# Performance work log

Hardware: AMD Instinct MI355X
Metric: run time of the kernel (lower is better)

Reference implementation:

```python
import jax, jax.numpy as jnp
import numpy as np

B, S, D, H = 2, 2048, 1024, 16
DH = D // H  # head_dim = 64


def setup_inputs() -> dict:
    key = jax.random.key(0)
    ks = jax.random.split(key, 10)
    inp = {
        "query": jax.random.normal(ks[0], (B, S, D), jnp.float32),
        "key": jax.random.normal(ks[1], (B, S, D), jnp.float32),
        "value": jax.random.normal(ks[2], (B, S, D), jnp.float32),
        "mask": jnp.ones((B, S), jnp.int32),
        # per-head q/k/v projections stacked over the head axis [H, D, DH]
        "Wq": jax.random.normal(ks[3], (H, D, DH), jnp.float32) * 0.02,
        "bq": jnp.zeros((H, DH), jnp.float32),
        "Wk": jax.random.normal(ks[4], (H, D, DH), jnp.float32) * 0.02,
        "bk": jnp.zeros((H, DH), jnp.float32),
        "Wv": jax.random.normal(ks[5], (H, D, DH), jnp.float32) * 0.02,
        "bv": jnp.zeros((H, DH), jnp.float32),
        # output projection fc: Linear(D, D)
        "Wo": jax.random.normal(ks[6], (D, D), jnp.float32) * 0.02,
        "bo": jnp.zeros((D,), jnp.float32),
    }
    return inp


def reference(query, key, value, mask, Wq, bq, Wk, bk, Wv, bv, Wo, bo):
    scale = 1.0 / jnp.sqrt(jnp.asarray(DH, query.dtype))
    # batched per-head projections: [B,S,D] x [H,D,DH] -> [B,H,S,DH]
    q = jnp.einsum('bsd,hde->bhse', query, Wq) + bq[None, :, None, :]
    k = jnp.einsum('bsd,hde->bhse', key, Wk) + bk[None, :, None, :]
    v = jnp.einsum('bsd,hde->bhse', value, Wv) + bv[None, :, None, :]
    # scaled dot-product attention scores [B,H,Sq,Sk]
    scores = jnp.einsum('bhqe,bhke->bhqk', q, k) * scale
    scores = jnp.where(mask[:, None, None, :] == 0, jnp.asarray(-1e9, scores.dtype), scores)
    attn = jax.nn.softmax(scores, axis=-1)
    ctx = jnp.einsum('bhqk,bhke->bhqe', attn, v)          # [B,H,S,DH]
    ctx = ctx.transpose(0, 2, 1, 3).reshape(query.shape[0], -1, H * DH)  # concat heads
    return ctx @ Wo + bo
```

## Files before the change

### kernel.cpp

```cpp
#include <hip/hip_runtime.h>
#include <stdint.h>
#include <math.h>


typedef __attribute__((ext_vector_type(8))) short short8;
typedef __attribute__((ext_vector_type(4))) float floatx4;

#define LOG2E 1.44269504088896340736f

__device__ __forceinline__ unsigned short f32_bf16(float f) {
  union { float f; unsigned u; } c; c.f = f;
  return (unsigned short)((c.u + 0x7FFFu + ((c.u >> 16) & 1u)) >> 16);
}
__device__ __forceinline__ float bf16_f32(unsigned short u) {
  union { unsigned u; float f; } c; c.u = ((unsigned)u) << 16;
  return c.f;
}
__device__ __forceinline__ void gld16(const void* g, void* l) {
  __builtin_amdgcn_global_load_lds((const __attribute__((address_space(1))) void*)g,
                                   (__attribute__((address_space(3))) void*)l, 16, 0, 0);
}


__global__ __launch_bounds__(256) void cvt3_kernel(
    const float* __restrict__ a, const float* __restrict__ b, const float* __restrict__ c,
    unsigned short* __restrict__ oa, unsigned short* __restrict__ ob, unsigned short* __restrict__ oc,
    const int* __restrict__ mask, float* __restrict__ mb, int n4) {
  int i = blockIdx.x * 256 + threadIdx.x;
  if (blockIdx.y == 0 && blockIdx.x < 16) {
    int j = blockIdx.x * 256 + threadIdx.x;
    mb[j] = (mask[j] == 0) ? (-1.0e9f * LOG2E) : 0.0f;
  }
  if (i >= n4) return;
  const float* in; unsigned short* out;
  if (blockIdx.y == 0) { in = a; out = oa; }
  else if (blockIdx.y == 1) { in = b; out = ob; }
  else { in = c; out = oc; }
  float4 v = reinterpret_cast<const float4*>(in)[i];
  ushort4 o;
  o.x = f32_bf16(v.x); o.y = f32_bf16(v.y); o.z = f32_bf16(v.z); o.w = f32_bf16(v.w);
  reinterpret_cast<ushort4*>(out)[i] = o;
}

__global__ __launch_bounds__(256) void transpose_w_kernel(
    const float* __restrict__ w0, const float* __restrict__ w1, const float* __restrict__ w2,
    const float* __restrict__ wo,
    unsigned short* __restrict__ o0, unsigned short* __restrict__ o1, unsigned short* __restrict__ o2,
    unsigned short* __restrict__ oo) {
  __shared__ float t[32][33];
  const int tx = threadIdx.x & 31, ty = threadIdx.x >> 5;
  const int zb = blockIdx.z;
  const float* in; unsigned short* out; int R, C, z, r0, c0;
  if (zb < 48) {
    if (blockIdx.y >= 2) return;
    const int sel = zb >> 4; z = zb & 15;
    in = (sel == 0) ? w0 : (sel == 1) ? w1 : w2;
    out = (sel == 0) ? o0 : (sel == 1) ? o1 : o2;
    R = 1024; C = 64;
  } else {
    in = wo; out = oo; R = 1024; C = 1024; z = 0;
  }
  r0 = blockIdx.x * 32; c0 = blockIdx.y * 32;
  const float* inp = in + (size_t)z * R * C;
  #pragma unroll
  for (int j = 0; j < 4; ++j)
    t[ty + j * 8][tx] = inp[(size_t)(r0 + ty + j * 8) * C + c0 + tx];
  __syncthreads();
  #pragma unroll
  for (int j = 0; j < 4; ++j)
    out[((size_t)z * C + c0 + ty + j * 8) * R + r0 + tx] = f32_bf16(t[tx][ty + j * 8]);
}


__device__ __forceinline__ void gemm_core(
    const unsigned short* __restrict__ A, const unsigned short* __restrict__ Bt,
    int K, int blockM, int blockN,
    unsigned short* As, unsigned short* Bs, floatx4 acc[4][4]) {
  const int tid = threadIdx.x;
  const int w = tid >> 6;
  const int lane = tid & 63;
  const int quad = lane >> 4, l15 = lane & 15;
  const int wm = w & 1, wn = w >> 1;
  const int srow = lane >> 2;
  const int scol = (lane & 3) * 8;

  #pragma unroll
  for (int mi = 0; mi < 4; ++mi)
    #pragma unroll
    for (int ni = 0; ni < 4; ++ni)
      acc[mi][ni] = (floatx4){0.f, 0.f, 0.f, 0.f};

  const unsigned short* Arow = A + (size_t)blockM * K;
  const unsigned short* Brow = Bt + (size_t)blockN * K;

  for (int k0 = 0; k0 < K; k0 += 32) {
    #pragma unroll
    for (int i = 0; i < 2; ++i) {
      int row = w * 32 + i * 16;
      gld16(Arow + (size_t)(row + srow) * K + k0 + scol, As + row * 32);
      gld16(Brow + (size_t)(row + srow) * K + k0 + scol, Bs + row * 32);
    }
    __syncthreads();
    short8 bf[4];
    #pragma unroll
    for (int ni = 0; ni < 4; ++ni)
      bf[ni] = *(const short8*)(Bs + (wn * 64 + ni * 16 + l15) * 32 + quad * 8);
    #pragma unroll
    for (int mi = 0; mi < 4; ++mi) {
      short8 af = *(const short8*)(As + (wm * 64 + mi * 16 + l15) * 32 + quad * 8);
      #pragma unroll
      for (int ni = 0; ni < 4; ++ni)
        acc[mi][ni] = __builtin_amdgcn_mfma_f32_16x16x32_bf16(af, bf[ni], acc[mi][ni], 0, 0, 0);
    }
    __syncthreads();
  }
}

__global__ __launch_bounds__(256) void gemm_proj_kernel(
    const unsigned short* __restrict__ qin, const unsigned short* __restrict__ kin,
    const unsigned short* __restrict__ vin,
    const unsigned short* __restrict__ WqT, const unsigned short* __restrict__ WkT,
    const unsigned short* __restrict__ WvT,
    const float* __restrict__ bq, const float* __restrict__ bk, const float* __restrict__ bv,
    unsigned short* __restrict__ Qp, unsigned short* __restrict__ Kp,
    unsigned short* __restrict__ Vt) {
  __shared__ unsigned short As[128 * 32];
  __shared__ unsigned short Bs[128 * 32];
  const int z = blockIdx.y, bx = blockIdx.x;
  const unsigned short *A, *Bt;
  const float* bias;
  int blockM, blockN;
  if (z < 2) {
    blockN = (bx & 7) * 128; blockM = (bx >> 3) * 128;
    A = z ? kin : qin; Bt = z ? WkT : WqT; bias = z ? bk : bq;
  } else {
    blockM = (bx & 7) * 128; blockN = (bx >> 3) * 128;
    A = WvT; Bt = vin; bias = bv;
  }
  floatx4 acc[4][4];
  gemm_core(A, Bt, 1024, blockM, blockN, As, Bs, acc);

  const int tid = threadIdx.x, w = tid >> 6, lane = tid & 63;
  const int quad = lane >> 4, l15 = lane & 15;
  const int wm = w & 1, wn = w >> 1;

  if (z < 2) {
    unsigned short* outp = z ? Kp : Qp;
    #pragma unroll
    for (int mi = 0; mi < 4; ++mi)
      #pragma unroll
      for (int ni = 0; ni < 4; ++ni) {
        const int n = blockN + wn * 64 + ni * 16 + l15;
        const int h = n >> 6, e = n & 63;
        const float bvv = bias[n];
        #pragma unroll
        for (int r = 0; r < 4; ++r) {
          const int m = blockM + wm * 64 + mi * 16 + quad * 4 + r;
          const int b = m >> 11, s = m & 2047;
          outp[(((size_t)b * 16 + h) * 2048 + s) * 64 + e] = f32_bf16(acc[mi][ni][r] + bvv);
        }
      }
  } else {
    #pragma unroll
    for (int mi = 0; mi < 4; ++mi) {
      float br[4];
      #pragma unroll
      for (int r = 0; r < 4; ++r)
        br[r] = bias[blockM + wm * 64 + mi * 16 + quad * 4 + r];
      #pragma unroll
      for (int ni = 0; ni < 4; ++ni) {
        const int n = blockN + wn * 64 + ni * 16 + l15;
        const int b = n >> 11, s = n & 2047;
        #pragma unroll
        for (int r = 0; r < 4; ++r) {
          const int m = blockM + wm * 64 + mi * 16 + quad * 4 + r;
          const int h = m >> 6, e = m & 63;
          Vt[(((size_t)b * 16 + h) * 64 + e) * 2048 + s] = f32_bf16(acc[mi][ni][r] + br[r]);
        }
      }
    }
  }
}

__global__ __launch_bounds__(256) void gemm_out_kernel(
    const unsigned short* __restrict__ A, const unsigned short* __restrict__ Bt,
    const float* __restrict__ bias, float* __restrict__ out, int K, int N) {
  __shared__ unsigned short As[128 * 32];
  __shared__ unsigned short Bs[64 * 32];
  const int tid = threadIdx.x;
  const int w = tid >> 6, lane = tid & 63;
  const int quad = lane >> 4, l15 = lane & 15;
  const int wm = w & 1, wn = w >> 1;
  const int srow = lane >> 2;
  const int scol = (lane & 3) * 8;
  const int blockN = blockIdx.x * 64, blockM = blockIdx.y * 128;

  floatx4 acc[4][2];
  #pragma unroll
  for (int mi = 0; mi < 4; ++mi)
    #pragma unroll
    for (int ni = 0; ni < 2; ++ni)
      acc[mi][ni] = (floatx4){0.f, 0.f, 0.f, 0.f};

  const unsigned short* Arow = A + (size_t)blockM * K;
  const unsigned short* Brow = Bt + (size_t)blockN * K;

  for (int k0 = 0; k0 < K; k0 += 32) {
    #pragma unroll
    for (int i = 0; i < 2; ++i) {
      int row = w * 32 + i * 16;
      gld16(Arow + (size_t)(row + srow) * K + k0 + scol, As + row * 32);
    }
    gld16(Brow + (size_t)(w * 16 + srow) * K + k0 + scol, Bs + (w * 16) * 32);
    __syncthreads();
    short8 bf[2];
    #pragma unroll
    for (int ni = 0; ni < 2; ++ni)
      bf[ni] = *(const short8*)(Bs + (wn * 32 + ni * 16 + l15) * 32 + quad * 8);
    #pragma unroll
    for (int mi = 0; mi < 4; ++mi) {
      short8 af = *(const short8*)(As + (wm * 64 + mi * 16 + l15) * 32 + quad * 8);
      #pragma unroll
      for (int ni = 0; ni < 2; ++ni)
        acc[mi][ni] = __builtin_amdgcn_mfma_f32_16x16x32_bf16(af, bf[ni], acc[mi][ni], 0, 0, 0);
    }
    __syncthreads();
  }

  #pragma unroll
  for (int mi = 0; mi < 4; ++mi)
    #pragma unroll
    for (int ni = 0; ni < 2; ++ni) {
      const int n = blockN + wn * 32 + ni * 16 + l15;
      const float bv = bias[n];
      #pragma unroll
      for (int r = 0; r < 4; ++r) {
        const int m = blockM + wm * 64 + mi * 16 + quad * 4 + r;
        out[(size_t)m * N + n] = acc[mi][ni][r] + bv;
      }
    }
}


__global__ __launch_bounds__(256, 3) void attn_kernel(
    const unsigned short* __restrict__ Q, const unsigned short* __restrict__ Kg,
    const unsigned short* __restrict__ Vt, const float* __restrict__ maskAdd,
    unsigned short* __restrict__ ctx) {
  const int S = 2048;
  const int tid = threadIdx.x;
  const int w = tid >> 6, lane = tid & 63, quad = lane >> 4, l15 = lane & 15;
  const int qb = blockIdx.x, bh = blockIdx.y;
  const int b = bh >> 4, h = bh & 15;
  const int q0 = qb * 128;

  __shared__ unsigned short Ks[128 * 64];
  __shared__ unsigned short Vs[64 * 128];
  __shared__ unsigned short Ps[4][32 * 64];
  unsigned short* Pw = Ps[w];

  const unsigned short* Qb = Q + (size_t)bh * S * 64;
  const unsigned short* Kb = Kg + (size_t)bh * S * 64;
  const unsigned short* Vb = Vt + (size_t)bh * 64 * S;
  const float* mb = maskAdd + (size_t)b * S;

  const float qs = 0.125f * LOG2E;
  short8 qf[2][2];
  #pragma unroll
  for (int mi = 0; mi < 2; ++mi)
    #pragma unroll
    for (int kq = 0; kq < 2; ++kq) {
      short8 v = *(const short8*)(Qb + (size_t)(q0 + w * 32 + mi * 16 + l15) * 64 + kq * 32 + quad * 8);
      #pragma unroll
      for (int j = 0; j < 8; ++j)
        v[j] = (short)f32_bf16(bf16_f32((unsigned short)v[j]) * qs);
      qf[mi][kq] = v;
    }

  short8 onesf;
  #pragma unroll
  for (int j = 0; j < 8; ++j) onesf[j] = (short)0x3F80;

  floatx4 O[2][4], ls[2];
  #pragma unroll
  for (int mi = 0; mi < 2; ++mi) {
    #pragma unroll
    for (int ne = 0; ne < 4; ++ne) O[mi][ne] = (floatx4){0.f, 0.f, 0.f, 0.f};
    ls[mi] = (floatx4){0.f, 0.f, 0.f, 0.f};
  }

  for (int t = 0; t < 16; ++t) {
    const int kv0 = t * 128;
    __syncthreads();
    #pragma unroll
    for (int i = 0; i < 4; ++i) {
      int r0 = w * 32 + i * 8;
      int row = r0 + (lane >> 3);
      int cg = (lane & 7) ^ (row & 7);
      gld16(Kb + (size_t)(kv0 + row) * 64 + cg * 8, Ks + r0 * 64);
    }
    #pragma unroll
    for (int i = 0; i < 4; ++i) {
      int r0 = w * 16 + i * 4;
      int row = r0 + (lane >> 4);
      int p = lane & 15;
      int cg = (p & 8) | ((p & 7) ^ (row & 7));
      gld16(Vb + (size_t)row * S + kv0 + cg * 8, Vs + r0 * 128);
    }
    float ma[8];
    #pragma unroll
    for (int ni = 0; ni < 8; ++ni) ma[ni] = mb[kv0 + ni * 16 + l15];
    __syncthreads();

    #pragma unroll
    for (int ph = 0; ph < 2; ++ph) {
      floatx4 sc[2][4];
      #pragma unroll
      for (int ni = 0; ni < 4; ++ni) {
        const int key = (ph * 4 + ni) * 16 + l15;
        short8 kf0 = *(const short8*)(Ks + key * 64 + ((quad) ^ (l15 & 7)) * 8);
        short8 kf1 = *(const short8*)(Ks + key * 64 + ((4 + quad) ^ (l15 & 7)) * 8);
        #pragma unroll
        for (int mi = 0; mi < 2; ++mi) {
          floatx4 s = (floatx4){0.f, 0.f, 0.f, 0.f};
          s = __builtin_amdgcn_mfma_f32_16x16x32_bf16(qf[mi][0], kf0, s, 0, 0, 0);
          s = __builtin_amdgcn_mfma_f32_16x16x32_bf16(qf[mi][1], kf1, s, 0, 0, 0);
          sc[mi][ni] = s;
        }
      }
      #pragma unroll
      for (int mi = 0; mi < 2; ++mi)
        #pragma unroll
        for (int r = 0; r < 4; ++r) {
          const int row = mi * 16 + quad * 4 + r;
          const int g = (row + (row >> 3)) & 7;
          #pragma unroll
          for (int ni = 0; ni < 4; ++ni) {
            float p = __builtin_amdgcn_exp2f(sc[mi][ni][r] + ma[ph * 4 + ni]);
            union { float f; unsigned u; } c; c.f = p;
            const int ch = (ni * 2 + (l15 >> 3)) ^ g;
            Pw[row * 64 + (ch & 7) * 8 + (l15 & 7)] = (unsigned short)(c.u >> 16);
          }
        }
      #pragma unroll
      for (int kkl = 0; kkl < 2; ++kkl) {
        const int kk = ph * 2 + kkl;
        short8 pfr[2], vf[4];
        #pragma unroll
        for (int mi = 0; mi < 2; ++mi) {
          const int gp = (2 * mi + l15 + (l15 >> 3)) & 7;
          pfr[mi] = *(const short8*)(Pw + (mi * 16 + l15) * 64 + ((kkl * 4 + quad) ^ gp) * 8);
        }
        #pragma unroll
        for (int ne = 0; ne < 4; ++ne) {
          const int c = kk * 4 + quad;
          vf[ne] = *(const short8*)(Vs + (ne * 16 + l15) * 128 + ((c & 8) | ((c & 7) ^ (l15 & 7))) * 8);
        }
        #pragma unroll
        for (int mi = 0; mi < 2; ++mi) {
          #pragma unroll
          for (int ne = 0; ne < 4; ++ne)
            O[mi][ne] = __builtin_amdgcn_mfma_f32_16x16x32_bf16(pfr[mi], vf[ne], O[mi][ne], 0, 0, 0);
          ls[mi] = __builtin_amdgcn_mfma_f32_16x16x32_bf16(pfr[mi], onesf, ls[mi], 0, 0, 0);
        }
      }
    }
  }

  #pragma unroll
  for (int mi = 0; mi < 2; ++mi)
    #pragma unroll
    for (int r = 0; r < 4; ++r) {
      const float inv = __builtin_amdgcn_rcpf(ls[mi][r]);
      const int s = q0 + w * 32 + mi * 16 + quad * 4 + r;
      #pragma unroll
      for (int ne = 0; ne < 4; ++ne)
        ctx[((size_t)b * S + s) * 1024 + h * 64 + ne * 16 + l15] = f32_bf16(O[mi][ne][r] * inv);
    }
}


extern "C" void kernel_launch(void* const* d_in, const int* in_sizes, int n_in,
                              void* d_out, int out_size, void* d_ws, size_t ws_size,
                              hipStream_t stream) {
  const float* query = (const float*)d_in[0];
  const float* key   = (const float*)d_in[1];
  const float* value = (const float*)d_in[2];
  const int*   mask  = (const int*)d_in[3];
  const float* Wq = (const float*)d_in[4];
  const float* bq = (const float*)d_in[5];
  const float* Wk = (const float*)d_in[6];
  const float* bk = (const float*)d_in[7];
  const float* Wv = (const float*)d_in[8];
  const float* bv = (const float*)d_in[9];
  const float* Wo = (const float*)d_in[10];
  const float* bo = (const float*)d_in[11];
  float* out = (float*)d_out;

  char* ws = (char*)d_ws;
  const size_t MB = 1024 * 1024;
  unsigned short* qin  = (unsigned short*)(ws + 0);
  unsigned short* kin  = (unsigned short*)(ws + 8 * MB);
  unsigned short* vin  = (unsigned short*)(ws + 16 * MB);
  unsigned short* WqT  = (unsigned short*)(ws + 24 * MB);
  unsigned short* WkT  = (unsigned short*)(ws + 26 * MB);
  unsigned short* WvT  = (unsigned short*)(ws + 28 * MB);
  unsigned short* WoT  = (unsigned short*)(ws + 30 * MB);
  unsigned short* Qp   = (unsigned short*)(ws + 32 * MB);
  unsigned short* Kp   = (unsigned short*)(ws + 40 * MB);
  unsigned short* Vt   = (unsigned short*)(ws + 48 * MB);
  float* maskAdd       = (float*)(ws + 56 * MB);
  unsigned short* ctxb = qin;

  cvt3_kernel<<<dim3(4096, 3), 256, 0, stream>>>(query, key, value, qin, kin, vin,
                                                 mask, maskAdd, 1048576);
  transpose_w_kernel<<<dim3(32, 32, 49), 256, 0, stream>>>(Wq, Wk, Wv, Wo, WqT, WkT, WvT, WoT);
  gemm_proj_kernel<<<dim3(256, 3), 256, 0, stream>>>(qin, kin, vin, WqT, WkT, WvT,
                                                     bq, bk, bv, Qp, Kp, Vt);
  attn_kernel<<<dim3(16, 32), 256, 0, stream>>>(Qp, Kp, Vt, maskAdd, ctxb);
  gemm_out_kernel<<<dim3(16, 32), 256, 0, stream>>>(ctxb, WoT, bo, out, 1024, 1024);
}
```

Before: 257.7 us.

## Double-buffer LDS tiles in GEMM and attention kernels to overlap loads

Converts the projection GEMM, output GEMM and attention KV loops to double-buffered shared memory. The next tile is issued with global_load_lds right after the barrier, and compute runs on the current buffer, with one barrier per iteration instead of two. The intent is to hide global-memory latency behind MFMA work. It doubles LDS use and drops the attention kernel's occupancy hint of 3 blocks per CU, which may lower occupancy.

After: 258.1 us. Within noise of the previous version (+0.1%).

```diff
diff --git a/kernel.cpp b/kernel.cpp
--- a/kernel.cpp
+++ b/kernel.cpp
@@ -90,29 +90,38 @@
     for (int ni = 0; ni < 4; ++ni)
       acc[mi][ni] = (floatx4){0.f, 0.f, 0.f, 0.f};
 
-  const unsigned short* Arow = A + (size_t)blockM * K;
-  const unsigned short* Brow = Bt + (size_t)blockN * K;
-
-  for (int k0 = 0; k0 < K; k0 += 32) {
+  const unsigned short* Arow = A + (size_t)blockM * K + (size_t)srow * K + scol;
+  const unsigned short* Brow = Bt + (size_t)blockN * K + (size_t)srow * K + scol;
+
+  auto stage = [&](int k0, int buf) {
+    unsigned short* Asb = As + buf * (128 * 32);
+    unsigned short* Bsb = Bs + buf * (128 * 32);
     #pragma unroll
     for (int i = 0; i < 2; ++i) {
       int row = w * 32 + i * 16;
-      gld16(Arow + (size_t)(row + srow) * K + k0 + scol, As + row * 32);
-      gld16(Brow + (size_t)(row + srow) * K + k0 + scol, Bs + row * 32);
-    }
+      gld16(Arow + (size_t)row * K + k0, Asb + row * 32);
+      gld16(Brow + (size_t)row * K + k0, Bsb + row * 32);
+    }
+  };
+
+  const int iters = K >> 5;
+  stage(0, 0);
+  for (int it = 0; it < iters; ++it) {
     __syncthreads();
+    if (it + 1 < iters) stage((it + 1) * 32, (it + 1) & 1);
+    const unsigned short* Asb = As + (it & 1) * (128 * 32);
+    const unsigned short* Bsb = Bs + (it & 1) * (128 * 32);
     short8 bf[4];
     #pragma unroll
     for (int ni = 0; ni < 4; ++ni)
-      bf[ni] = *(const short8*)(Bs + (wn * 64 + ni * 16 + l15) * 32 + quad * 8);
+      bf[ni] = *(const short8*)(Bsb + (wn * 64 + ni * 16 + l15) * 32 + quad * 8);
     #pragma unroll
     for (int mi = 0; mi < 4; ++mi) {
-      short8 af = *(const short8*)(As + (wm * 64 + mi * 16 + l15) * 32 + quad * 8);
+      short8 af = *(const short8*)(Asb + (wm * 64 + mi * 16 + l15) * 32 + quad * 8);
       #pragma unroll
       for (int ni = 0; ni < 4; ++ni)
         acc[mi][ni] = __builtin_amdgcn_mfma_f32_16x16x32_bf16(af, bf[ni], acc[mi][ni], 0, 0, 0);
     }
-    __syncthreads();
   }
 }
 
@@ -124,8 +133,8 @@
     const float* __restrict__ bq, const float* __restrict__ bk, const float* __restrict__ bv,
     unsigned short* __restrict__ Qp, unsigned short* __restrict__ Kp,
     unsigned short* __restrict__ Vt) {
-  __shared__ unsigned short As[128 * 32];
-  __shared__ unsigned short Bs[128 * 32];
+  __shared__ unsigned short As[2][128 * 32];
+  __shared__ unsigned short Bs[2][128 * 32];
   const int z = blockIdx.y, bx = blockIdx.x;
   const unsigned short *A, *Bt;
   const float* bias;
@@ -138,7 +147,7 @@
     A = WvT; Bt = vin; bias = bv;
   }
   floatx4 acc[4][4];
-  gemm_core(A, Bt, 1024, blockM, blockN, As, Bs, acc);
+  gemm_core(A, Bt, 1024, blockM, blockN, As[0], Bs[0], acc);
 
   const int tid = threadIdx.x, w = tid >> 6, lane = tid & 63;
   const int quad = lane >> 4, l15 = lane & 15;
@@ -185,8 +194,8 @@
 __global__ __launch_bounds__(256) void gemm_out_kernel(
     const unsigned short* __restrict__ A, const unsigned short* __restrict__ Bt,
     const float* __restrict__ bias, float* __restrict__ out, int K, int N) {
-  __shared__ unsigned short As[128 * 32];
-  __shared__ unsigned short Bs[64 * 32];
+  __shared__ unsigned short As[2][128 * 32];
+  __shared__ unsigned short Bs[2][64 * 32];
   const int tid = threadIdx.x;
   const int w = tid >> 6, lane = tid & 63;
   const int quad = lane >> 4, l15 = lane & 15;
@@ -202,29 +211,36 @@
     for (int ni = 0; ni < 2; ++ni)
       acc[mi][ni] = (floatx4){0.f, 0.f, 0.f, 0.f};
 
-  const unsigned short* Arow = A + (size_t)blockM * K;
-  const unsigned short* Brow = Bt + (size_t)blockN * K;
-
-  for (int k0 = 0; k0 < K; k0 += 32) {
+  const unsigned short* Arow = A + (size_t)blockM * K + (size_t)srow * K + scol;
+  const unsigned short* Brow = Bt + (size_t)blockN * K + (size_t)srow * K + scol;
+
+  auto stage = [&](int k0, int buf) {
     #pragma unroll
     for (int i = 0; i < 2; ++i) {
       int row = w * 32 + i * 16;
-      gld16(Arow + (size_t)(row + srow) * K + k0 + scol, As + row * 32);
-    }
-    gld16(Brow + (size_t)(w * 16 + srow) * K + k0 + scol, Bs + (w * 16) * 32);
+      gld16(Arow + (size_t)row * K + k0, As[buf] + row * 32);
+    }
+    gld16(Brow + (size_t)(w * 16) * K + k0, Bs[buf] + (w * 16) * 32);
+  };
+
+  const int iters = K >> 5;
+  stage(0, 0);
+  for (int it = 0; it < iters; ++it) {
     __syncthreads();
+    if (it + 1 < iters) stage((it + 1) * 32, (it + 1) & 1);
+    const unsigned short* Asb = As[it & 1];
+    const unsigned short* Bsb = Bs[it & 1];
     short8 bf[2];
     #pragma unroll
     for (int ni = 0; ni < 2; ++ni)
-      bf[ni] = *(const short8*)(Bs + (wn * 32 + ni * 16 + l15) * 32 + quad * 8);
+      bf[ni] = *(const short8*)(Bsb + (wn * 32 + ni * 16 + l15) * 32 + quad * 8);
     #pragma unroll
     for (int mi = 0; mi < 4; ++mi) {
-      short8 af = *(const short8*)(As + (wm * 64 + mi * 16 + l15) * 32 + quad * 8);
+      short8 af = *(const short8*)(Asb + (wm * 64 + mi * 16 + l15) * 32 + quad * 8);
       #pragma unroll
       for (int ni = 0; ni < 2; ++ni)
         acc[mi][ni] = __builtin_amdgcn_mfma_f32_16x16x32_bf16(af, bf[ni], acc[mi][ni], 0, 0, 0);
     }
-    __syncthreads();
   }
 
   #pragma unroll
@@ -242,7 +258,7 @@
 }
 
 
-__global__ __launch_bounds__(256, 3) void attn_kernel(
+__global__ __launch_bounds__(256) void attn_kernel(
     const unsigned short* __restrict__ Q, const unsigned short* __restrict__ Kg,
     const unsigned short* __restrict__ Vt, const float* __restrict__ maskAdd,
     unsigned short* __restrict__ ctx) {
@@ -253,8 +269,8 @@
   const int b = bh >> 4, h = bh & 15;
   const int q0 = qb * 128;
 
-  __shared__ unsigned short Ks[128 * 64];
-  __shared__ unsigned short Vs[64 * 128];
+  __shared__ unsigned short Ks[2][128 * 64];
+  __shared__ unsigned short Vs[2][64 * 128];
   __shared__ unsigned short Ps[4][32 * 64];
   unsigned short* Pw = Ps[w];
 
@@ -288,15 +304,14 @@
     ls[mi] = (floatx4){0.f, 0.f, 0.f, 0.f};
   }
 
-  for (int t = 0; t < 16; ++t) {
+  auto stage_kv = [&](int t, int buf) {
     const int kv0 = t * 128;
-    __syncthreads();
     #pragma unroll
     for (int i = 0; i < 4; ++i) {
       int r0 = w * 32 + i * 8;
       int row = r0 + (lane >> 3);
       int cg = (lane & 7) ^ (row & 7);
-      gld16(Kb + (size_t)(kv0 + row) * 64 + cg * 8, Ks + r0 * 64);
+      gld16(Kb + (size_t)(kv0 + row) * 64 + cg * 8, Ks[buf] + r0 * 64);
     }
     #pragma unroll
     for (int i = 0; i < 4; ++i) {
@@ -304,12 +319,20 @@
       int row = r0 + (lane >> 4);
       int p = lane & 15;
       int cg = (p & 8) | ((p & 7) ^ (row & 7));
-      gld16(Vb + (size_t)row * S + kv0 + cg * 8, Vs + r0 * 128);
-    }
+      gld16(Vb + (size_t)row * S + kv0 + cg * 8, Vs[buf] + r0 * 128);
+    }
+  };
+
+  stage_kv(0, 0);
+  for (int t = 0; t < 16; ++t) {
+    const int kv0 = t * 128;
+    __syncthreads();
     float ma[8];
     #pragma unroll
     for (int ni = 0; ni < 8; ++ni) ma[ni] = mb[kv0 + ni * 16 + l15];
-    __syncthreads();
+    if (t + 1 < 16) stage_kv(t + 1, (t + 1) & 1);
+    const unsigned short* Ksb = Ks[t & 1];
+    const unsigned short* Vsb = Vs[t & 1];
 
     #pragma unroll
     for (int ph = 0; ph < 2; ++ph) {
@@ -317,8 +340,8 @@
       #pragma unroll
       for (int ni = 0; ni < 4; ++ni) {
         const int key = (ph * 4 + ni) * 16 + l15;
-        short8 kf0 = *(const short8*)(Ks + key * 64 + ((quad) ^ (l15 & 7)) * 8);
-        short8 kf1 = *(const short8*)(Ks + key * 64 + ((4 + quad) ^ (l15 & 7)) * 8);
+        short8 kf0 = *(const short8*)(Ksb + key * 64 + ((quad) ^ (l15 & 7)) * 8);
+        short8 kf1 = *(const short8*)(Ksb + key * 64 + ((4 + quad) ^ (l15 & 7)) * 8);
         #pragma unroll
         for (int mi = 0; mi < 2; ++mi) {
           floatx4 s = (floatx4){0.f, 0.f, 0.f, 0.f};
@@ -353,7 +376,7 @@
         #pragma unroll
         for (int ne = 0; ne < 4; ++ne) {
           const int c = kk * 4 + quad;
-          vf[ne] = *(const short8*)(Vs + (ne * 16 + l15) * 128 + ((c & 8) | ((c & 7) ^ (l15 & 7))) * 8);
+          vf[ne] = *(const short8*)(Vsb + (ne * 16 + l15) * 128 + ((c & 8) | ((c & 7) ^ (l15 & 7))) * 8);
         }
         #pragma unroll
         for (int mi = 0; mi < 2; ++mi) {
```
